# Performance work log

Measured on AMD Instinct MI355X. Metric: run time of the kernel, lower is better.

The kernel has to match this reference:

```python
import jax, jax.numpy as jnp
import numpy as np
import math

J = 4096          # input_output_size
B = 4096          # batch
S = 4             # n_samples
PI = 0.5          # mixture weight
SIGMA1 = 1.0
SIGMA2 = 0.002
RHO_SCALE = -5.0
MU_SCALE = math.sqrt(6.0 / J)
LOG_SQRT_2PI = 0.5 * math.log(2.0 * math.pi)


def _normal_logpdf(x, mu, sigma):
    # elementwise Normal log-density
    return -LOG_SQRT_2PI - jnp.log(sigma) - (x - mu) ** 2 / (2.0 * sigma ** 2)


def setup_inputs() -> dict:
    key = jax.random.key(0)
    k1, k2, k3 = jax.random.split(key, 3)
    x = jax.random.normal(k1, (B, J), dtype=jnp.float32)
    weight_mu = jax.random.uniform(k2, (J,), dtype=jnp.float32,
                                   minval=-MU_SCALE, maxval=MU_SCALE)
    weight_rho = jnp.full((J,), RHO_SCALE, dtype=jnp.float32)
    eps = jax.random.normal(k3, (S, J), dtype=jnp.float32)
    return {"x": x, "weight_mu": weight_mu, "weight_rho": weight_rho,
            "eps": eps, "n_samples": S}


def reference(x, weight_mu, weight_rho, eps, n_samples):
    # reparameterized weight sample: [S, J]
    sigma = jnp.log1p(jnp.exp(weight_rho))            # softplus, [J]
    weight = weight_mu + sigma * eps                  # [S, J]

    # variational posterior log-prob: sum over samples and features
    log_variational_posterior = jnp.sum(_normal_logpdf(weight, weight_mu, sigma))

    # scale-mixture Gaussian prior log-prob (stable via logaddexp)
    lp1 = _normal_logpdf(weight, 0.0, jnp.float32(SIGMA1)) + jnp.log(jnp.float32(PI))
    lp2 = _normal_logpdf(weight, 0.0, jnp.float32(SIGMA2)) + jnp.log(jnp.float32(1.0 - PI))
    log_prior = jnp.sum(jnp.logaddexp(lp1, lp2))

    # einsum('bj,jk->bjk', w, eye) then einsum('bij,bjk->bik', x, .)
    # is mathematically out[s,b,j] = x[b,j] * weight[s,j]
    out = x[None, :, :] * weight[:, None, :]          # [S, B, J]
    return out, log_prior, log_variational_posterior
```

## Files before the change

### kernel.cpp

```cpp
#include <hip/hip_runtime.h>
#include <math.h>

#define LOG_SQRT_2PI 0.9189385332046727f

__global__ __launch_bounds__(1024)
void bel_prep_reduce(const float* __restrict__ mu,
                     const float* __restrict__ rho,
                     const float* __restrict__ eps,
                     float* __restrict__ weight,
                     float* __restrict__ out_scalars,
                     int S, int J) {
    const int n = S * J;
    double acc_lvp = 0.0;
    double acc_lpr = 0.0;

    const float log_half = logf(0.5f);
    const float log_sigma2 = logf(0.002f);
    const float inv_2s2_2 = 1.0f / (2.0f * 0.002f * 0.002f);

    for (int idx = threadIdx.x; idx < n; idx += blockDim.x) {
        const int j = idx % J;
        const float m = mu[j];
        const float r = rho[j];
        const float e = eps[idx];

        const float sigma = log1pf(expf(r));
        const float w = m + sigma * e;
        weight[idx] = w;

        const float d = w - m;
        acc_lvp += (double)(-LOG_SQRT_2PI - logf(sigma)
                            - (d * d) / (2.0f * sigma * sigma));

        const float w2 = w * w;
        const float lp1 = -LOG_SQRT_2PI - 0.5f * w2 + log_half;
        const float lp2 = -LOG_SQRT_2PI - log_sigma2 - w2 * inv_2s2_2 + log_half;
        const float mx = fmaxf(lp1, lp2);
        const float mn = fminf(lp1, lp2);
        acc_lpr += (double)(mx + log1pf(expf(mn - mx)));
    }

    for (int off = 32; off > 0; off >>= 1) {
        acc_lvp += __shfl_down(acc_lvp, off, 64);
        acc_lpr += __shfl_down(acc_lpr, off, 64);
    }

    __shared__ double s_lvp[16];
    __shared__ double s_lpr[16];
    const int wid = threadIdx.x >> 6;
    const int lane = threadIdx.x & 63;
    if (lane == 0) { s_lvp[wid] = acc_lvp; s_lpr[wid] = acc_lpr; }
    __syncthreads();
    if (threadIdx.x == 0) {
        double lvp = 0.0, lpr = 0.0;
        const int nw = blockDim.x >> 6;
        for (int i = 0; i < nw; ++i) { lvp += s_lvp[i]; lpr += s_lpr[i]; }
        out_scalars[0] = (float)lpr;
        out_scalars[1] = (float)lvp;
    }
}

__global__ __launch_bounds__(256)
void bel_scale(const float4* __restrict__ x4,
               const float4* __restrict__ w4,
               float4* __restrict__ o4,
               long long total4,
               int Jv,
               int S) {
    long long idx = (long long)blockIdx.x * blockDim.x + threadIdx.x;
    const long long stride = (long long)gridDim.x * blockDim.x;
    for (; idx < total4; idx += stride) {
        const int jv = (int)(idx % Jv);
        const float4 xv = x4[idx];
        #pragma unroll 4
        for (int s = 0; s < S; ++s) {
            const float4 wv = w4[(long long)s * Jv + jv];
            float4 ov;
            ov.x = xv.x * wv.x;
            ov.y = xv.y * wv.y;
            ov.z = xv.z * wv.z;
            ov.w = xv.w * wv.w;
            o4[(long long)s * total4 + idx] = ov;
        }
    }
}

extern "C" void kernel_launch(void* const* d_in, const int* in_sizes, int n_in,
                              void* d_out, int out_size, void* d_ws, size_t ws_size,
                              hipStream_t stream) {
    const float* x   = (const float*)d_in[0];
    const float* mu  = (const float*)d_in[1];
    const float* rho = (const float*)d_in[2];
    const float* eps = (const float*)d_in[3];

    const int J = in_sizes[1];
    const int B = in_sizes[0] / J;
    const int S = in_sizes[3] / J;

    float* out = (float*)d_out;
    float* weight = (float*)d_ws;
    float* out_scalars = out + (long long)S * B * J;

    bel_prep_reduce<<<1, 1024, 0, stream>>>(mu, rho, eps, weight, out_scalars, S, J);

    const long long total4 = (long long)B * J / 4;
    const int Jv = J / 4;
    const int block = 256;
    long long blocks = (total4 + block - 1) / block;
    if (blocks > 65535LL * 64) blocks = 65535LL * 64;
    bel_scale<<<(int)blocks, block, 0, stream>>>(
        (const float4*)x, (const float4*)weight, (float4*)out, total4, Jv, S);
}
```

Baseline: 360.7 us.

## Fuse weight sampling and log-prob reduction into a single scaling kernel

```diff
diff --git a/kernel.cpp b/kernel.cpp
--- a/kernel.cpp
+++ b/kernel.cpp
@@ -3,85 +3,150 @@
 
 #define LOG_SQRT_2PI 0.9189385332046727f
 
-__global__ __launch_bounds__(1024)
-void bel_prep_reduce(const float* __restrict__ mu,
-                     const float* __restrict__ rho,
-                     const float* __restrict__ eps,
-                     float* __restrict__ weight,
-                     float* __restrict__ out_scalars,
-                     int S, int J) {
+typedef float f32x4 __attribute__((ext_vector_type(4)));
+
+__device__ __forceinline__
+void reduce_duty(const float* __restrict__ mu,
+                 const float* __restrict__ rho,
+                 const float* __restrict__ eps,
+                 float* __restrict__ out_scalars,
+                 double* __restrict__ ws,
+                 int S, int J, int nRed)
+{
     const int n = S * J;
-    double acc_lvp = 0.0;
-    double acc_lpr = 0.0;
+    double lvp = 0.0, lpr = 0.0;
+    const float log_half   = -0.6931471805599453f;
+    const float log_sigma2 = -6.214608098422191f;
+    const float inv_2s2_2  = 125000.0f;
 
-    const float log_half = logf(0.5f);
-    const float log_sigma2 = logf(0.002f);
-    const float inv_2s2_2 = 1.0f / (2.0f * 0.002f * 0.002f);
-
-    for (int idx = threadIdx.x; idx < n; idx += blockDim.x) {
+    for (int idx = blockIdx.x * blockDim.x + threadIdx.x; idx < n;
+         idx += nRed * blockDim.x) {
         const int j = idx % J;
         const float m = mu[j];
         const float r = rho[j];
         const float e = eps[idx];
-
-        const float sigma = log1pf(expf(r));
-        const float w = m + sigma * e;
-        weight[idx] = w;
+        const float sg = log1pf(expf(r));
+        const float w  = m + sg * e;
 
         const float d = w - m;
-        acc_lvp += (double)(-LOG_SQRT_2PI - logf(sigma)
-                            - (d * d) / (2.0f * sigma * sigma));
+        lvp += (double)(-LOG_SQRT_2PI - logf(sg) - (d * d) / (2.0f * sg * sg));
 
-        const float w2 = w * w;
+        const float w2  = w * w;
         const float lp1 = -LOG_SQRT_2PI - 0.5f * w2 + log_half;
         const float lp2 = -LOG_SQRT_2PI - log_sigma2 - w2 * inv_2s2_2 + log_half;
-        const float mx = fmaxf(lp1, lp2);
-        const float mn = fminf(lp1, lp2);
-        acc_lpr += (double)(mx + log1pf(expf(mn - mx)));
+        const float mx  = fmaxf(lp1, lp2);
+        const float mn  = fminf(lp1, lp2);
+        lpr += (double)(mx + log1pf(expf(mn - mx)));
     }
 
     for (int off = 32; off > 0; off >>= 1) {
-        acc_lvp += __shfl_down(acc_lvp, off, 64);
-        acc_lpr += __shfl_down(acc_lpr, off, 64);
+        lvp += __shfl_down(lvp, off, 64);
+        lpr += __shfl_down(lpr, off, 64);
     }
-
-    __shared__ double s_lvp[16];
-    __shared__ double s_lpr[16];
-    const int wid = threadIdx.x >> 6;
-    const int lane = threadIdx.x & 63;
-    if (lane == 0) { s_lvp[wid] = acc_lvp; s_lpr[wid] = acc_lpr; }
+    __shared__ double s_l[2][4];
+    const int wid = threadIdx.x >> 6, lane = threadIdx.x & 63;
+    if (lane == 0) { s_l[0][wid] = lvp; s_l[1][wid] = lpr; }
     __syncthreads();
     if (threadIdx.x == 0) {
-        double lvp = 0.0, lpr = 0.0;
         const int nw = blockDim.x >> 6;
-        for (int i = 0; i < nw; ++i) { lvp += s_lvp[i]; lpr += s_lpr[i]; }
-        out_scalars[0] = (float)lpr;
-        out_scalars[1] = (float)lvp;
+        double bl_lvp = 0.0, bl_lpr = 0.0;
+        for (int i = 0; i < nw; ++i) { bl_lvp += s_l[0][i]; bl_lpr += s_l[1][i]; }
+        atomicAdd(&ws[0], bl_lpr);
+        atomicAdd(&ws[1], bl_lvp);
+        __threadfence();
+        unsigned int* counter = (unsigned int*)(ws + 2);
+        const unsigned int prev = atomicAdd(counter, 1u);
+        if (prev == (unsigned)(nRed - 1)) {
+            __threadfence();
+            out_scalars[0] = (float)atomicAdd(&ws[0], 0.0);
+            out_scalars[1] = (float)atomicAdd(&ws[1], 0.0);
+        }
     }
 }
 
 __global__ __launch_bounds__(256)
-void bel_scale(const float4* __restrict__ x4,
-               const float4* __restrict__ w4,
-               float4* __restrict__ o4,
-               long long total4,
-               int Jv,
-               int S) {
+void bel_fused4(const f32x4* __restrict__ x4,
+                const float* __restrict__ mu,
+                const float* __restrict__ rho,
+                const float* __restrict__ eps,
+                f32x4* __restrict__ o4,
+                float* __restrict__ out_scalars,
+                double* __restrict__ ws,
+                int B, int J, int jblocks, int nRed)
+{
+    if ((int)blockIdx.x < nRed)
+        reduce_duty(mu, rho, eps, out_scalars, ws, 4, J, nRed);
+
+    const int Jv      = J >> 2;
+    const int jb      = blockIdx.x % jblocks;
+    const int bstart  = blockIdx.x / jblocks;
+    const int bstride = gridDim.x / jblocks;
+    const int jv      = jb * blockDim.x + threadIdx.x;
+    if (jv >= Jv) return;
+
+    const f32x4 muv  = ((const f32x4*)mu)[jv];
+    const f32x4 rhov = ((const f32x4*)rho)[jv];
+    f32x4 sg;
+    sg.x = log1pf(expf(rhov.x));
+    sg.y = log1pf(expf(rhov.y));
+    sg.z = log1pf(expf(rhov.z));
+    sg.w = log1pf(expf(rhov.w));
+
+    const f32x4 e0 = ((const f32x4*)eps)[0 * Jv + jv];
+    const f32x4 e1 = ((const f32x4*)eps)[1 * Jv + jv];
+    const f32x4 e2 = ((const f32x4*)eps)[2 * Jv + jv];
+    const f32x4 e3 = ((const f32x4*)eps)[3 * Jv + jv];
+
+    const f32x4 w0 = muv + sg * e0;
+    const f32x4 w1 = muv + sg * e1;
+    const f32x4 w2 = muv + sg * e2;
+    const f32x4 w3 = muv + sg * e3;
+
+    const size_t plane = (size_t)B * Jv;
+
+    #pragma unroll 4
+    for (int b = bstart; b < B; b += bstride) {
+        const size_t rb = (size_t)b * Jv + jv;
+        const f32x4 xv = x4[rb];
+        __builtin_nontemporal_store(xv * w0, &o4[0 * plane + rb]);
+        __builtin_nontemporal_store(xv * w1, &o4[1 * plane + rb]);
+        __builtin_nontemporal_store(xv * w2, &o4[2 * plane + rb]);
+        __builtin_nontemporal_store(xv * w3, &o4[3 * plane + rb]);
+    }
+}
+
+__global__ __launch_bounds__(256)
+void bel_reduce_gen(const float* __restrict__ mu, const float* __restrict__ rho,
+                    const float* __restrict__ eps, float* __restrict__ out_scalars,
+                    double* __restrict__ ws, int S, int J, int nRed)
+{
+    reduce_duty(mu, rho, eps, out_scalars, ws, S, J, nRed);
+}
+
+__global__ __launch_bounds__(256)
+void bel_scale_gen(const f32x4* __restrict__ x4,
+                   const float* __restrict__ mu, const float* __restrict__ rho,
+                   const float* __restrict__ eps, f32x4* __restrict__ o4,
+                   long long total4, int Jv, int B, int S)
+{
     long long idx = (long long)blockIdx.x * blockDim.x + threadIdx.x;
     const long long stride = (long long)gridDim.x * blockDim.x;
-    for (; idx < total4; idx += stride) {
-        const int jv = (int)(idx % Jv);
-        const float4 xv = x4[idx];
-        #pragma unroll 4
-        for (int s = 0; s < S; ++s) {
-            const float4 wv = w4[(long long)s * Jv + jv];
-            float4 ov;
-            ov.x = xv.x * wv.x;
-            ov.y = xv.y * wv.y;
-            ov.z = xv.z * wv.z;
-            ov.w = xv.w * wv.w;
-            o4[(long long)s * total4 + idx] = ov;
-        }
+    const long long plane = (long long)B * Jv;
+    for (; idx < (long long)S * plane; idx += stride) {
+        const int s  = (int)(idx / plane);
+        const long long r = idx % plane;
+        const int jv = (int)(r % Jv);
+        const f32x4 muv  = ((const f32x4*)mu)[jv];
+        const f32x4 rhov = ((const f32x4*)rho)[jv];
+        const f32x4 ev   = ((const f32x4*)eps)[(long long)s * Jv + jv];
+        const f32x4 xv   = x4[r];
+        f32x4 sg;
+        sg.x = log1pf(expf(rhov.x));
+        sg.y = log1pf(expf(rhov.y));
+        sg.z = log1pf(expf(rhov.z));
+        sg.w = log1pf(expf(rhov.w));
+        const f32x4 ov = xv * (muv + sg * ev);
+        __builtin_nontemporal_store(ov, &o4[idx]);
     }
 }
 
@@ -98,16 +163,28 @@
     const int S = in_sizes[3] / J;
 
     float* out = (float*)d_out;
-    float* weight = (float*)d_ws;
-    float* out_scalars = out + (long long)S * B * J;
+    float* out_scalars = out + (size_t)S * B * J;
+    double* ws = (double*)d_ws;
 
-    bel_prep_reduce<<<1, 1024, 0, stream>>>(mu, rho, eps, weight, out_scalars, S, J);
+    (void)hipMemsetAsync(d_ws, 0, 24, stream);
 
-    const long long total4 = (long long)B * J / 4;
+    const int nRed = 32;
+    const int block = 256;
     const int Jv = J / 4;
-    const int block = 256;
-    long long blocks = (total4 + block - 1) / block;
-    if (blocks > 65535LL * 64) blocks = 65535LL * 64;
-    bel_scale<<<(int)blocks, block, 0, stream>>>(
-        (const float4*)x, (const float4*)weight, (float4*)out, total4, Jv, S);
+
+    if (S == 4 && (Jv % block) == 0) {
+        const int jblocks  = Jv / block;
+        const int bstride  = (B < 1024) ? B : 1024;
+        const int grid     = jblocks * bstride;
+        bel_fused4<<<grid, block, 0, stream>>>(
+            (const f32x4*)x, mu, rho, eps, (f32x4*)out, out_scalars, ws,
+            B, J, jblocks, nRed);
+    } else {
+        bel_reduce_gen<<<nRed, block, 0, stream>>>(mu, rho, eps, out_scalars, ws, S, J, nRed);
+        const long long total4 = (long long)S * B * Jv;
+        long long blocks = (total4 + block - 1) / block;
+        if (blocks > 2048) blocks = 2048;
+        bel_scale_gen<<<(int)blocks, block, 0, stream>>>(
+            (const f32x4*)x, mu, rho, eps, (f32x4*)out, total4, Jv, B, S);
+    }
 }
```

Measured after the change: 336.5 us. 6.7% less time.
